# Kernel optimization log

Measured on AMD Instinct MI355X. Metric: run time of the kernel, lower is better.

Reference implementation:

```python
import jax, jax.numpy as jnp
import numpy as np
from jax import lax

B, CIN, H, W = 16, 256, 64, 64
DP = 512          # displace_planes
COUT = 256        # outplanes
NUM_OFFSET = 64   # displace_planes // BIND_CHAN(8)
K = 5             # DPOOL_SIZE (odd)
EPS = float(np.finfo(np.float32).eps)
BN_EPS = 1e-5
EXP_CLAMP = 88.722835


def conv1x1(x, w, b):
    # x: [B,C,H,W], w: [O,C], b: [O]
    return jnp.einsum('bchw,oc->bohw', x, w) + b[None, :, None, None]


def batchnorm(x, gamma, beta):
    m = x.mean(axis=(0, 2, 3))
    v = x.var(axis=(0, 2, 3))
    inv = lax.rsqrt(v + BN_EPS)
    return (x - m[None, :, None, None]) * (inv * gamma)[None, :, None, None] + beta[None, :, None, None]


def dynamic_pool(x, sigma):
    # per-channel Gaussian depthwise conv in exp space, back to log space
    r = (jnp.arange(K) - K // 2).astype(jnp.float32)
    dissq = r[:, None] ** 2 + r[None, :] ** 2                     # [K,K]
    kern = jnp.exp(-(dissq / 2.0)[None] / (sigma ** 2 + EPS)[:, None, None])  # [C,K,K]
    kern = kern / kern.sum(axis=(1, 2), keepdims=True)
    expx = jnp.exp(jnp.minimum(x, EXP_CLAMP))
    out = lax.conv_general_dilated(
        expx, kern[:, None],                                      # rhs [C,1,K,K]
        window_strides=(1, 1), padding=[(K // 2, K // 2)] * 2,
        dimension_numbers=('NCHW', 'OIHW', 'NCHW'),
        feature_group_count=DP)
    return jnp.log(out + EPS)


def displace(feat, offsets):
    # feat: [B,C,H,W]; offsets: [NUM_OFFSET,2] (dy,dx), each bound to C//NUM_OFFSET channels.
    # Per-channel uniform bilinear shift with zero padding outside the map.
    Bn, C, Hn, Wn = feat.shape
    chan = C // NUM_OFFSET
    dy = jnp.repeat(offsets[:, 0], chan)  # [C]
    dx = jnp.repeat(offsets[:, 1], chan)
    y0 = jnp.floor(dy); x0 = jnp.floor(dx)
    fy = dy - y0; fx = dx - x0            # fractional parts (diff. wrt offsets)
    y0i = y0.astype(jnp.int32); x0i = x0.astype(jnp.int32)
    rows = jnp.arange(Hn); cols = jnp.arange(Wn)

    def one_chan(img, y0c, x0c, fyc, fxc):
        # img: [B,H,W]; shift is separable per row/col since offset is uniform
        def shifted(oy, ox):
            ry = rows + y0c + oy
            rx = cols + x0c + ox
            my = (ry >= 0) & (ry < Hn)
            mx = (rx >= 0) & (rx < Wn)
            g = img[:, jnp.clip(ry, 0, Hn - 1), :][:, :, jnp.clip(rx, 0, Wn - 1)]
            return g * (my[:, None] & mx[None, :]).astype(img.dtype)[None]
        return ((1 - fyc) * (1 - fxc) * shifted(0, 0)
                + (1 - fyc) * fxc * shifted(0, 1)
                + fyc * (1 - fxc) * shifted(1, 0)
                + fyc * fxc * shifted(1, 1))

    return jax.vmap(one_chan, in_axes=(1, 0, 0, 0, 0), out_axes=1)(feat, y0i, x0i, fy, fx)


def attention(x, w, b, gamma, beta):
    a = conv1x1(x, w, b)
    a = batchnorm(a, gamma, beta)
    a = jax.nn.softplus(a)
    # SpaceNormalization: normalize over spatial dims
    return a / a.sum(axis=(2, 3), keepdims=True)


def setup_inputs() -> dict:
    key = jax.random.key(0)
    ks = jax.random.split(key, 6)
    return {
        'x': jax.random.normal(ks[0], (B, CIN, H, W), jnp.float32),
        'pre_w': jax.random.normal(ks[1], (DP, CIN), jnp.float32) / np.sqrt(CIN),
        'pre_b': jnp.zeros((DP,), jnp.float32),
        'sigma': jnp.full((DP,), K / 2 / 2, jnp.float32),
        'offsets': jax.random.normal(ks[2], (NUM_OFFSET, 2), jnp.float32) * 3.0,
        'atten_w': jax.random.normal(ks[3], (DP, CIN), jnp.float32) / np.sqrt(CIN),
        'atten_b': jnp.zeros((DP,), jnp.float32),
        'atten_gamma': jnp.ones((DP,), jnp.float32),
        'atten_beta': jnp.zeros((DP,), jnp.float32),
        'post_w': jax.random.normal(ks[4], (COUT, DP), jnp.float32) / np.sqrt(DP),
        'post_b': jnp.zeros((COUT,), jnp.float32),
        'bn_gamma': jnp.ones((COUT,), jnp.float32),
        'bn_beta': jnp.zeros((COUT,), jnp.float32),
    }


def reference(x, pre_w, pre_b, sigma, offsets, atten_w, atten_b, atten_gamma,
              atten_beta, post_w, post_b, bn_gamma, bn_beta):
    out_pre = conv1x1(x, pre_w, pre_b)                 # [B,DP,H,W]
    out_pre = dynamic_pool(out_pre, sigma)
    out_dis = displace(out_pre, offsets)
    out_atten = attention(x, atten_w, atten_b, atten_gamma, atten_beta)
    out_post = conv1x1(out_atten * out_dis, post_w, post_b)  # [B,COUT,H,W]
    out_skip = x + out_post                            # inplanes==outplanes, stride=1
    return jax.nn.relu(batchnorm(out_skip, bn_gamma, bn_beta))
```

## Files before the change

kernel.cpp:

```cpp
#include <hip/hip_runtime.h>
#include <cmath>

#define NB   16
#define CINC 256
#define DPC  512
#define COUTC 256
#define HWS  4096
#define EPSF 1.1920928955078125e-07f
#define BN_EPS 1e-5f
#define EXP_CLAMP 88.722835f
#define TS 76
#define PS2 66

typedef unsigned int uint32;
typedef unsigned short ushort;
typedef __bf16 bf16x8 __attribute__((ext_vector_type(8)));
typedef float f32x4 __attribute__((ext_vector_type(4)));
typedef unsigned short ushort8 __attribute__((ext_vector_type(8)));

__device__ inline ushort f2bf(float f) {
    __bf16 h = (__bf16)f;
    return __builtin_bit_cast(ushort, h);
}
__device__ inline float bf2f(ushort u) {
    return __builtin_bit_cast(float, (uint32)u << 16);
}
__device__ inline float softplus_fast(float v) {
    return fmaxf(v, 0.f) + __logf(1.f + __expf(-fabsf(v)));
}
__device__ __forceinline__ void gload16(const void* g, void* l) {
    __builtin_amdgcn_global_load_lds(
        (__attribute__((address_space(1))) void*)g,
        (__attribute__((address_space(3))) void*)l, 16, 0, 0);
}
__device__ __forceinline__ void hard_barrier() {
    __builtin_amdgcn_sched_barrier(0);
    __builtin_amdgcn_s_barrier();
    __builtin_amdgcn_sched_barrier(0);
}

template<int OTOT, int KTOT, bool DUALBIAS, bool PARTIALS>
__global__ __launch_bounds__(256) void mfma_gemm_k(
    const ushort* __restrict__ A, const ushort* __restrict__ BT,
    const float* __restrict__ bias1, const float* __restrict__ bias2,
    const float* __restrict__ skip, ushort* __restrict__ outp,
    float* __restrict__ part_s, float* __restrict__ part_s2) {
    const int hw0 = blockIdx.x * 128;
    const int o0  = blockIdx.y * 256;
    const int b   = blockIdx.z;
    __shared__ ushort As[2][256 * 32];
    __shared__ ushort Bs[2][128 * 32];
    const int tid  = threadIdx.x;
    const int lane = tid & 63;
    const int w    = tid >> 6;
    const int wm0  = (w >> 1) * 128;
    const int wn0  = (w & 1) * 64;

    f32x4 acc[8][4] = {};

    const ushort* Ab = A + (size_t)o0 * KTOT;
    const ushort* Bb = BT + ((size_t)b * HWS + hw0) * KTOT;
    const int rsub  = lane >> 2;
    const int ksubp = ((lane & 3) ^ ((lane >> 3) & 3)) * 8;

    auto stage = [&](int buf, int k0) {
#pragma unroll
        for (int i = 0; i < 4; ++i) {
            const int row = w * 64 + i * 16 + rsub;
            gload16(Ab + (size_t)row * KTOT + k0 + ksubp, &As[buf][(w * 64 + i * 16) * 32]);
        }
#pragma unroll
        for (int i = 0; i < 2; ++i) {
            const int row = w * 32 + i * 16 + rsub;
            gload16(Bb + (size_t)row * KTOT + k0 + ksubp, &Bs[buf][(w * 32 + i * 16) * 32]);
        }
    };

    constexpr int NSTEP = KTOT / 32;
    stage(0, 0);
    stage(1, 32);
    int cur = 0;
    for (int step = 0; step < NSTEP; ++step) {
        if (step == NSTEP - 1) asm volatile("s_waitcnt vmcnt(0)" ::: "memory");
        else                   asm volatile("s_waitcnt vmcnt(6)" ::: "memory");
        hard_barrier();
        bf16x8 af[8], bfr[4];
#pragma unroll
        for (int mi = 0; mi < 8; ++mi) {
            int row = wm0 + mi * 16 + (lane & 15);
            int sl = (lane >> 4) ^ ((row >> 1) & 3);
            af[mi] = *reinterpret_cast<const bf16x8*>(&As[cur][row * 32 + sl * 8]);
        }
#pragma unroll
        for (int ni = 0; ni < 4; ++ni) {
            int row = wn0 + ni * 16 + (lane & 15);
            int sl = (lane >> 4) ^ ((row >> 1) & 3);
            bfr[ni] = *reinterpret_cast<const bf16x8*>(&Bs[cur][row * 32 + sl * 8]);
        }
#pragma unroll
        for (int mi = 0; mi < 8; ++mi)
#pragma unroll
            for (int ni = 0; ni < 4; ++ni)
                acc[mi][ni] = __builtin_amdgcn_mfma_f32_16x16x32_bf16(
                    af[mi], bfr[ni], acc[mi][ni], 0, 0, 0);
        hard_barrier();
        if (step + 2 < NSTEP) stage(cur, (step + 2) * 32);
        cur ^= 1;
    }

    float* pS  = reinterpret_cast<float*>(&As[0][0]);
    float* pS2 = pS + 512;
    if constexpr (PARTIALS) __syncthreads();

#pragma unroll
    for (int mi = 0; mi < 8; ++mi) {
#pragma unroll
        for (int r = 0; r < 4; ++r) {
            int chL = wm0 + mi * 16 + ((lane >> 4) << 2) + r;
            int o = o0 + chL;
            float bi;
            if constexpr (DUALBIAS) bi = (o < 512) ? bias1[o] : bias2[o - 512];
            else bi = bias1[o];
            size_t base = ((size_t)b * OTOT + o) * HWS + hw0 + wn0 + (lane & 15);
            float s1 = 0.f, s2 = 0.f;
#pragma unroll
            for (int ni = 0; ni < 4; ++ni) {
                float v = acc[mi][ni][r] + bi;
                if constexpr (PARTIALS) v += skip[base + ni * 16];
                ushort tb = f2bf(v);
                outp[base + ni * 16] = tb;
                if constexpr (PARTIALS) {
                    float vf = bf2f(tb);
                    s1 += vf; s2 += vf * vf;
                }
            }
            if constexpr (PARTIALS) {
#pragma unroll
                for (int off = 1; off <= 8; off <<= 1) {
                    s1 += __shfl_xor(s1, off, 64);
                    s2 += __shfl_xor(s2, off, 64);
                }
                if ((lane & 15) == 0) {
                    pS[(w & 1) * 256 + chL]  = s1;
                    pS2[(w & 1) * 256 + chL] = s2;
                }
            }
        }
    }
    if constexpr (PARTIALS) {
        __syncthreads();
        if (tid < 256) {
            int k = blockIdx.x * NB + b;
            float S  = pS[tid]  + pS[256 + tid];
            float S2 = pS2[tid] + pS2[256 + tid];
            part_s[(size_t)(o0 + tid) * 512 + k]  = S;
            part_s2[(size_t)(o0 + tid) * 512 + k] = S2;
        }
    }
}

__global__ __launch_bounds__(256) void castT_k(const float* __restrict__ x,
                                               ushort* __restrict__ xT) {
    const int b = blockIdx.z, c0 = blockIdx.y * 64, hw0 = blockIdx.x * 64;
    __shared__ float tile[64][65];
    const int tid = threadIdx.x;
#pragma unroll
    for (int r = 0; r < 16; ++r) {
        int cl = r * 4 + (tid >> 6), hwl = tid & 63;
        tile[cl][hwl] = x[((size_t)b * CINC + c0 + cl) * HWS + hw0 + hwl];
    }
    __syncthreads();
#pragma unroll
    for (int r = 0; r < 16; ++r) {
        int hwl = r * 4 + (tid >> 6), cl = tid & 63;
        xT[((size_t)b * HWS + hw0 + hwl) * CINC + c0 + cl] = f2bf(tile[cl][hwl]);
    }
}

__global__ __launch_bounds__(256) void cast_k(const float* __restrict__ in,
                                              ushort* __restrict__ out, int n) {
    int i = (blockIdx.x * 256 + threadIdx.x) * 4;
    if (i < n) {
        float4 v = *reinterpret_cast<const float4*>(in + i);
        out[i + 0] = f2bf(v.x); out[i + 1] = f2bf(v.y);
        out[i + 2] = f2bf(v.z); out[i + 3] = f2bf(v.w);
    }
}

__global__ __launch_bounds__(512, 8) void pooldisp_k(ushort* __restrict__ dp,
                                                     const float* __restrict__ sigma,
                                                     const float* __restrict__ offsets) {
    const int bc = blockIdx.x;
    const int b = bc >> 9, c = bc & 511;
    __shared__ float  tmp[68 * TS];
    __shared__ ushort pl[64 * PS2];
    const int tid = threadIdx.x;
    ushort* ip = dp + ((size_t)b * 1024 + c) * HWS;

    float s = sigma[c];
    float inv = 0.5f / (s * s + EPSF);
    float g0 = __expf(-4.f * inv), g1 = __expf(-1.f * inv);
    float gs = g0 + g1 + 1.f + g1 + g0;
    float rnorm = 1.f / (gs * gs);

    {
        int r4 = tid >> 7, col = tid & 127;
        if (col < TS) {
            int row = (r4 < 2) ? r4 : 64 + r4;
            tmp[row * TS + col] = 0.f;
        }
    }
    {
        int hr = tid >> 3, w0 = (tid & 7) * 8;
        const ushort* rp = ip + hr * 64 + w0;
        ushort8 mv = *reinterpret_cast<const ushort8*>(rp);
        float e[12];
        e[0] = (w0 > 0) ? __expf(fminf(bf2f(rp[-2]), EXP_CLAMP)) : 0.f;
        e[1] = (w0 > 0) ? __expf(fminf(bf2f(rp[-1]), EXP_CLAMP)) : 0.f;
#pragma unroll
        for (int q = 0; q < 8; ++q)
            e[2 + q] = __expf(fminf(bf2f(mv[q]), EXP_CLAMP));
        e[10] = (w0 < 56) ? __expf(fminf(bf2f(rp[8]), EXP_CLAMP)) : 0.f;
        e[11] = (w0 < 56) ? __expf(fminf(bf2f(rp[9]), EXP_CLAMP)) : 0.f;
        f32x4 o0, o1;
#pragma unroll
        for (int j = 0; j < 4; ++j) {
            o0[j] = g0 * (e[j] + e[j + 4]) + g1 * (e[j + 1] + e[j + 3]) + e[j + 2];
            o1[j] = g0 * (e[j + 4] + e[j + 8]) + g1 * (e[j + 5] + e[j + 7]) + e[j + 6];
        }
        *reinterpret_cast<f32x4*>(&tmp[(hr + 2) * TS + w0]) = o0;
        *reinterpret_cast<f32x4*>(&tmp[(hr + 2) * TS + w0 + 4]) = o1;
    }
    __syncthreads();

#pragma unroll
    for (int t = 0; t < 2; ++t) {
        int task = tid + t * 512;
        int h = task >> 4, wq = (task & 15) * 4;
        f32x4 t0 = *reinterpret_cast<const f32x4*>(&tmp[(h + 0) * TS + wq]);
        f32x4 t1 = *reinterpret_cast<const f32x4*>(&tmp[(h + 1) * TS + wq]);
        f32x4 t2 = *reinterpret_cast<const f32x4*>(&tmp[(h + 2) * TS + wq]);
        f32x4 t3 = *reinterpret_cast<const f32x4*>(&tmp[(h + 3) * TS + wq]);
        f32x4 t4 = *reinterpret_cast<const f32x4*>(&tmp[(h + 4) * TS + wq]);
        ushort o[4];
#pragma unroll
        for (int j = 0; j < 4; ++j) {
            float v = g0 * (t0[j] + t4[j]) + g1 * (t1[j] + t3[j]) + t2[j];
            o[j] = f2bf(__logf(v * rnorm + EPSF));
        }
        *reinterpret_cast<uint32*>(&pl[h * PS2 + wq]) =
            (uint32)o[0] | ((uint32)o[1] << 16);
        *reinterpret_cast<uint32*>(&pl[h * PS2 + wq + 2]) =
            (uint32)o[2] | ((uint32)o[3] << 16);
    }
    __syncthreads();

    {
        int oi = c >> 3;
        float dy = offsets[oi * 2 + 0];
        float dx = offsets[oi * 2 + 1];
        float y0f = floorf(dy), x0f = floorf(dx);
        float fy = dy - y0f, fx = dx - x0f;
        int y0 = (int)y0f, x0 = (int)x0f;
        float w00 = (1.f - fy) * (1.f - fx), w01 = (1.f - fy) * fx;
        float w10 = fy * (1.f - fx),         w11 = fy * fx;
        int h = tid >> 3, w = (tid & 7) * 8;
        int ry0 = h + y0, ry1 = ry0 + 1;
        bool my0 = (ry0 >= 0) & (ry0 < 64);
        bool my1 = (ry1 >= 0) & (ry1 < 64);
        float e0[9], e1[9];
#pragma unroll
        for (int j = 0; j < 9; ++j) {
            int col = w + x0 + j;
            bool mx = (col >= 0) & (col < 64);
            e0[j] = (my0 & mx) ? bf2f(pl[ry0 * PS2 + col]) : 0.f;
            e1[j] = (my1 & mx) ? bf2f(pl[ry1 * PS2 + col]) : 0.f;
        }
        ushort8 ov;
#pragma unroll
        for (int q = 0; q < 8; ++q)
            ov[q] = f2bf(w00 * e0[q] + w01 * e0[q + 1]
                       + w10 * e1[q] + w11 * e1[q + 1]);
        *reinterpret_cast<ushort8*>(ip + tid * 8) = ov;
    }
}

__global__ __launch_bounds__(1024) void attstats_k(const ushort* __restrict__ dp,
                                                   const float* __restrict__ gamma,
                                                   const float* __restrict__ beta,
                                                   float* __restrict__ scale,
                                                   float* __restrict__ shift,
                                                   float* __restrict__ rsum) {
    const int c = blockIdx.x;
    const int t = threadIdx.x;
    const int wv = t >> 6, lane = t & 63;
    const ushort* p = dp + ((size_t)wv * 1024 + 512 + c) * HWS;

    ushort8 v[8];
    float s = 0.f, s2 = 0.f;
#pragma unroll
    for (int k = 0; k < 8; ++k) {
        v[k] = *reinterpret_cast<const ushort8*>(p + lane * 8 + k * 512);
#pragma unroll
        for (int j = 0; j < 8; ++j) { float f = bf2f(v[k][j]); s += f; s2 += f * f; }
    }
#pragma unroll
    for (int off = 32; off > 0; off >>= 1) {
        s += __shfl_down(s, off, 64);
        s2 += __shfl_down(s2, off, 64);
    }
    __shared__ float t1[16], t2[16], scsh[2];
    if (lane == 0) { t1[wv] = s; t2[wv] = s2; }
    __syncthreads();
    if (t == 0) {
        float S = 0.f, S2 = 0.f;
#pragma unroll
        for (int k = 0; k < 16; ++k) { S += t1[k]; S2 += t2[k]; }
        float n = (float)(NB * HWS);
        float mean = S / n;
        float var = S2 / n - mean * mean;
        float invs = rsqrtf(var + BN_EPS);
        float sc = invs * gamma[c];
        float sh = beta[c] - mean * sc;
        scale[c] = sc; shift[c] = sh;
        scsh[0] = sc; scsh[1] = sh;
    }
    __syncthreads();
    float sc = scsh[0], sh = scsh[1];
    float ps = 0.f;
#pragma unroll
    for (int k = 0; k < 8; ++k)
#pragma unroll
        for (int j = 0; j < 8; ++j)
            ps += softplus_fast(bf2f(v[k][j]) * sc + sh);
#pragma unroll
    for (int off = 32; off > 0; off >>= 1) ps += __shfl_down(ps, off, 64);
    if (lane == 0) rsum[wv * DPC + c] = 1.f / ps;
}

__global__ __launch_bounds__(256) void attmulT_k(const ushort* __restrict__ dp,
                                                 const float* __restrict__ scale,
                                                 const float* __restrict__ shift,
                                                 const float* __restrict__ rsum,
                                                 ushort* __restrict__ mT) {
    const int b = blockIdx.z, c0 = blockIdx.y * 64, hw0 = blockIdx.x * 64;
    __shared__ float tile[64][65];
    const int tid = threadIdx.x;
#pragma unroll
    for (int r = 0; r < 16; ++r) {
        int cl = r * 4 + (tid >> 6), hwl = tid & 63;
        int c = c0 + cl;
        size_t aidx = ((size_t)b * 1024 + 512 + c) * HWS + hw0 + hwl;
        size_t didx = ((size_t)b * 1024 + c) * HWS + hw0 + hwl;
        float a = bf2f(dp[aidx]) * scale[c] + shift[c];
        float m = softplus_fast(a) * rsum[b * DPC + c] * bf2f(dp[didx]);
        tile[cl][hwl] = m;
    }
    __syncthreads();
#pragma unroll
    for (int r = 0; r < 16; ++r) {
        int hwl = r * 4 + (tid >> 6), cl = tid & 63;
        mT[((size_t)b * HWS + hw0 + hwl) * DPC + c0 + cl] = f2bf(tile[cl][hwl]);
    }
}

__global__ __launch_bounds__(256) void bnred_k(const float* __restrict__ part_s,
                                               const float* __restrict__ part_s2,
                                               const float* __restrict__ gamma,
                                               const float* __restrict__ beta,
                                               float* __restrict__ scale,
                                               float* __restrict__ shift) {
    const int c = blockIdx.x, t = threadIdx.x;
    float s  = part_s[(size_t)c * 512 + t]  + part_s[(size_t)c * 512 + 256 + t];
    float s2 = part_s2[(size_t)c * 512 + t] + part_s2[(size_t)c * 512 + 256 + t];
#pragma unroll
    for (int off = 32; off > 0; off >>= 1) {
        s += __shfl_down(s, off, 64);
        s2 += __shfl_down(s2, off, 64);
    }
    __shared__ float t1[4], t2[4];
    int lane = t & 63, wid = t >> 6;
    if (lane == 0) { t1[wid] = s; t2[wid] = s2; }
    __syncthreads();
    if (t == 0) {
        float S = t1[0] + t1[1] + t1[2] + t1[3];
        float S2 = t2[0] + t2[1] + t2[2] + t2[3];
        float n = (float)(NB * HWS);
        float mean = S / n;
        float var = S2 / n - mean * mean;
        float invs = rsqrtf(var + BN_EPS);
        float sc = invs * gamma[c];
        scale[c] = sc;
        shift[c] = beta[c] - mean * sc;
    }
}

__global__ __launch_bounds__(256) void final_k(const ushort* __restrict__ t,
                                               const float* __restrict__ scale,
                                               const float* __restrict__ shift,
                                               float* __restrict__ out) {
    int i = (blockIdx.x * 256 + threadIdx.x) * 8;
    int c = (i >> 12) & (COUTC - 1);
    float sc = scale[c], sh = shift[c];
    ushort8 v = *reinterpret_cast<const ushort8*>(t + i);
    float4 a, b4;
#pragma unroll
    for (int j = 0; j < 4; ++j) a[j] = fmaxf(bf2f(v[j]) * sc + sh, 0.f);
#pragma unroll
    for (int j = 0; j < 4; ++j) b4[j] = fmaxf(bf2f(v[4 + j]) * sc + sh, 0.f);
    *reinterpret_cast<float4*>(out + i) = a;
    *reinterpret_cast<float4*>(out + i + 4) = b4;
}

extern "C" void kernel_launch(void* const* d_in, const int* in_sizes, int n_in,
                              void* d_out, int out_size, void* d_ws, size_t ws_size,
                              hipStream_t stream) {
    const float* x           = (const float*)d_in[0];
    const float* pre_w       = (const float*)d_in[1];
    const float* pre_b       = (const float*)d_in[2];
    const float* sigma       = (const float*)d_in[3];
    const float* offsets     = (const float*)d_in[4];
    const float* atten_w     = (const float*)d_in[5];
    const float* atten_b     = (const float*)d_in[6];
    const float* atten_gamma = (const float*)d_in[7];
    const float* atten_beta  = (const float*)d_in[8];
    const float* post_w      = (const float*)d_in[9];
    const float* post_b      = (const float*)d_in[10];
    const float* bn_gamma    = (const float*)d_in[11];
    const float* bn_beta     = (const float*)d_in[12];
    float* out = (float*)d_out;

    char* wsb = (char*)d_ws;
    ushort* xT     = (ushort*)(wsb);
    ushort* wbig   = (ushort*)(wsb + ((size_t)32 << 20));
    ushort* wpost  = wbig + 1024 * 256;
    float*  stats  = (float*)(wsb + ((size_t)33 << 20));
    ushort* dpout  = (ushort*)(wsb + ((size_t)34 << 20));
    ushort* tbuf   = dpout;
    ushort* mT     = (ushort*)(wsb + ((size_t)162 << 20));
    float*  part_s  = (float*)(wsb + ((size_t)226 << 20));
    float*  part_s2 = part_s + 256 * 512;

    float* scaleA = stats;
    float* shiftA = stats + 512;
    float* rsum   = stats + 1024;
    float* scale2 = stats + 9216;
    float* shift2 = stats + 9472;

    castT_k<<<dim3(64, 4, NB), 256, 0, stream>>>(x, xT);
    cast_k<<<128, 256, 0, stream>>>(pre_w,   wbig,             DPC * CINC);
    cast_k<<<128, 256, 0, stream>>>(atten_w, wbig + 512 * 256, DPC * CINC);
    cast_k<<<128, 256, 0, stream>>>(post_w,  wpost,            COUTC * DPC);

    mfma_gemm_k<1024, CINC, true, false><<<dim3(32, 4, NB), 256, 0, stream>>>(
        wbig, xT, pre_b, atten_b, nullptr, dpout, nullptr, nullptr);
    pooldisp_k<<<NB * DPC, 512, 0, stream>>>(dpout, sigma, offsets);
    attstats_k<<<DPC, 1024, 0, stream>>>(dpout, atten_gamma, atten_beta,
                                         scaleA, shiftA, rsum);
    attmulT_k<<<dim3(64, 8, NB), 256, 0, stream>>>(dpout, scaleA, shiftA, rsum, mT);
    mfma_gemm_k<COUTC, DPC, false, true><<<dim3(32, 1, NB), 256, 0, stream>>>(
        wpost, mT, post_b, post_b, x, tbuf, part_s, part_s2);
    bnred_k<<<COUTC, 256, 0, stream>>>(part_s, part_s2, bn_gamma, bn_beta,
                                       scale2, shift2);
    final_k<<<(NB * COUTC * HWS) / 2048, 256, 0, stream>>>(tbuf, scale2, shift2, out);
}
```

Baseline: 264.7 us.

## Fuse input transpose/cast into first GEMM via register-staged fp32 loads

Removes the separate castT_k kernel, which transposed x into a bf16 HW-major buffer. The first GEMM now reads fp32 x directly, converts it to bf16 in registers and writes it swizzled into LDS. The pipeline also changes from a two-stage async global_load_lds prefetch with vmcnt waits to issue-next/compute/commit with two __syncthreads per step. This affects the second GEMM too. The aim is to save a kernel launch and a full write and read of the transposed activation, at the cost of strided fp32 global loads and a shallower prefetch.

```diff
diff --git a/kernel.cpp b/kernel.cpp
--- a/kernel.cpp
+++ b/kernel.cpp
@@ -33,15 +33,10 @@
         (__attribute__((address_space(1))) void*)g,
         (__attribute__((address_space(3))) void*)l, 16, 0, 0);
 }
-__device__ __forceinline__ void hard_barrier() {
-    __builtin_amdgcn_sched_barrier(0);
-    __builtin_amdgcn_s_barrier();
-    __builtin_amdgcn_sched_barrier(0);
-}
-
-template<int OTOT, int KTOT, bool DUALBIAS, bool PARTIALS>
+
+template<int OTOT, int KTOT, bool DUALBIAS, bool PARTIALS, bool XF32>
 __global__ __launch_bounds__(256) void mfma_gemm_k(
-    const ushort* __restrict__ A, const ushort* __restrict__ BT,
+    const ushort* __restrict__ A, const void* __restrict__ Bsrc,
     const float* __restrict__ bias1, const float* __restrict__ bias2,
     const float* __restrict__ skip, ushort* __restrict__ outp,
     float* __restrict__ part_s, float* __restrict__ part_s2) {
@@ -59,31 +54,60 @@
     f32x4 acc[8][4] = {};
 
     const ushort* Ab = A + (size_t)o0 * KTOT;
-    const ushort* Bb = BT + ((size_t)b * HWS + hw0) * KTOT;
     const int rsub  = lane >> 2;
     const int ksubp = ((lane & 3) ^ ((lane >> 3) & 3)) * 8;
 
-    auto stage = [&](int buf, int k0) {
+    const int hwl = tid & 127;
+    const int cs0 = tid >> 7;
+    const float* xrow = XF32 ? ((const float*)Bsrc + (size_t)b * KTOT * HWS + hw0 + hwl)
+                             : nullptr;
+    const ushort* BbT = XF32 ? nullptr
+                             : ((const ushort*)Bsrc + ((size_t)b * HWS + hw0) * KTOT);
+
+    float breg[2][8];
+
+    auto stage_issue = [&](int buf, int k0) {
 #pragma unroll
         for (int i = 0; i < 4; ++i) {
             const int row = w * 64 + i * 16 + rsub;
             gload16(Ab + (size_t)row * KTOT + k0 + ksubp, &As[buf][(w * 64 + i * 16) * 32]);
         }
-#pragma unroll
-        for (int i = 0; i < 2; ++i) {
-            const int row = w * 32 + i * 16 + rsub;
-            gload16(Bb + (size_t)row * KTOT + k0 + ksubp, &Bs[buf][(w * 32 + i * 16) * 32]);
+        if constexpr (XF32) {
+#pragma unroll
+            for (int sg = 0; sg < 2; ++sg) {
+                const int cb = k0 + (cs0 + sg * 2) * 8;
+#pragma unroll
+                for (int j = 0; j < 8; ++j)
+                    breg[sg][j] = xrow[(size_t)(cb + j) * HWS];
+            }
+        } else {
+#pragma unroll
+            for (int i = 0; i < 2; ++i) {
+                const int row = w * 32 + i * 16 + rsub;
+                gload16(BbT + (size_t)row * KTOT + k0 + ksubp, &Bs[buf][(w * 32 + i * 16) * 32]);
+            }
         }
     };
+    auto stage_commit = [&](int buf) {
+        if constexpr (XF32) {
+#pragma unroll
+            for (int sg = 0; sg < 2; ++sg) {
+                ushort8 u;
+#pragma unroll
+                for (int j = 0; j < 8; ++j) u[j] = f2bf(breg[sg][j]);
+                const int phys = (cs0 + sg * 2) ^ ((hwl >> 1) & 3);
+                *reinterpret_cast<ushort8*>(&Bs[buf][hwl * 32 + phys * 8]) = u;
+            }
+        }
+    };
 
     constexpr int NSTEP = KTOT / 32;
-    stage(0, 0);
-    stage(1, 32);
+    stage_issue(0, 0);
+    stage_commit(0);
+    __syncthreads();
     int cur = 0;
     for (int step = 0; step < NSTEP; ++step) {
-        if (step == NSTEP - 1) asm volatile("s_waitcnt vmcnt(0)" ::: "memory");
-        else                   asm volatile("s_waitcnt vmcnt(6)" ::: "memory");
-        hard_barrier();
+        if (step + 1 < NSTEP) stage_issue(cur ^ 1, (step + 1) * 32);
         bf16x8 af[8], bfr[4];
 #pragma unroll
         for (int mi = 0; mi < 8; ++mi) {
@@ -103,14 +127,14 @@
             for (int ni = 0; ni < 4; ++ni)
                 acc[mi][ni] = __builtin_amdgcn_mfma_f32_16x16x32_bf16(
                     af[mi], bfr[ni], acc[mi][ni], 0, 0, 0);
-        hard_barrier();
-        if (step + 2 < NSTEP) stage(cur, (step + 2) * 32);
+        __syncthreads();
+        if (step + 1 < NSTEP) stage_commit(cur ^ 1);
+        __syncthreads();
         cur ^= 1;
     }
 
     float* pS  = reinterpret_cast<float*>(&As[0][0]);
     float* pS2 = pS + 512;
-    if constexpr (PARTIALS) __syncthreads();
 
 #pragma unroll
     for (int mi = 0; mi < 8; ++mi) {
@@ -156,24 +180,6 @@
             part_s[(size_t)(o0 + tid) * 512 + k]  = S;
             part_s2[(size_t)(o0 + tid) * 512 + k] = S2;
         }
-    }
-}
-
-__global__ __launch_bounds__(256) void castT_k(const float* __restrict__ x,
-                                               ushort* __restrict__ xT) {
-    const int b = blockIdx.z, c0 = blockIdx.y * 64, hw0 = blockIdx.x * 64;
-    __shared__ float tile[64][65];
-    const int tid = threadIdx.x;
-#pragma unroll
-    for (int r = 0; r < 16; ++r) {
-        int cl = r * 4 + (tid >> 6), hwl = tid & 63;
-        tile[cl][hwl] = x[((size_t)b * CINC + c0 + cl) * HWS + hw0 + hwl];
-    }
-    __syncthreads();
-#pragma unroll
-    for (int r = 0; r < 16; ++r) {
-        int hwl = r * 4 + (tid >> 6), cl = tid & 63;
-        xT[((size_t)b * HWS + hw0 + hwl) * CINC + c0 + cl] = f2bf(tile[cl][hwl]);
     }
 }
 
@@ -431,7 +437,6 @@
     float* out = (float*)d_out;
 
     char* wsb = (char*)d_ws;
-    ushort* xT     = (ushort*)(wsb);
     ushort* wbig   = (ushort*)(wsb + ((size_t)32 << 20));
     ushort* wpost  = wbig + 1024 * 256;
     float*  stats  = (float*)(wsb + ((size_t)33 << 20));
@@ -447,18 +452,17 @@
     float* scale2 = stats + 9216;
     float* shift2 = stats + 9472;
 
-    castT_k<<<dim3(64, 4, NB), 256, 0, stream>>>(x, xT);
     cast_k<<<128, 256, 0, stream>>>(pre_w,   wbig,             DPC * CINC);
     cast_k<<<128, 256, 0, stream>>>(atten_w, wbig + 512 * 256, DPC * CINC);
     cast_k<<<128, 256, 0, stream>>>(post_w,  wpost,            COUTC * DPC);
 
-    mfma_gemm_k<1024, CINC, true, false><<<dim3(32, 4, NB), 256, 0, stream>>>(
-        wbig, xT, pre_b, atten_b, nullptr, dpout, nullptr, nullptr);
+    mfma_gemm_k<1024, CINC, true, false, true><<<dim3(32, 4, NB), 256, 0, stream>>>(
+        wbig, x, pre_b, atten_b, nullptr, dpout, nullptr, nullptr);
     pooldisp_k<<<NB * DPC, 512, 0, stream>>>(dpout, sigma, offsets);
     attstats_k<<<DPC, 1024, 0, stream>>>(dpout, atten_gamma, atten_beta,
                                          scaleA, shiftA, rsum);
     attmulT_k<<<dim3(64, 8, NB), 256, 0, stream>>>(dpout, scaleA, shiftA, rsum, mT);
-    mfma_gemm_k<COUTC, DPC, false, true><<<dim3(32, 1, NB), 256, 0, stream>>>(
+    mfma_gemm_k<COUTC, DPC, false, true, false><<<dim3(32, 1, NB), 256, 0, stream>>>(
         wpost, mT, post_b, post_b, x, tbuf, part_s, part_s2);
     bnred_k<<<COUTC, 256, 0, stream>>>(part_s, part_s2, bn_gamma, bn_beta,
                                        scale2, shift2);
```

After: 267.3 us. Within noise of the previous version (+1.0%).
